# Kernel tuning notes

Measured on AMD Instinct MI355X. Metric: run time of the kernel, lower is better.

## Reference

```python
import jax, jax.numpy as jnp
import numpy as np

B, L, D, T = 32, 2048, 64, 512          # batch, seq_len, input_dim, pred steps
H, EK = 2, 64                           # num_heads, embed_dim_per_head
E = H * EK                              # embed_dim = 128
P = 2                                   # function 'L' -> 2 coefficients
LAT, HID = 64, 64                       # latent_dim, hidden_dim
DIM = 2 * D                             # value dim after cat(X, M)


def setup_inputs() -> dict:
    key = jax.random.key(0)
    ks = jax.random.split(key, 20)
    s = 0.05
    inp = {
        "timesteps": jnp.sort(jax.random.uniform(ks[0], (B, L)), axis=-1),
        "X": jax.random.normal(ks[1], (B, L, D)),
        "M": jax.random.bernoulli(ks[2], 0.5, (B, L, D)).astype(jnp.float32),
        "y_time_steps": jnp.sort(jax.random.uniform(ks[3], (B, T)), axis=-1),
        # time_embedding: Linear(1, E)
        "te_w": jax.random.normal(ks[4], (1, E)) * s,
        "te_b": jax.random.normal(ks[5], (E,)) * s,
        # learned queries (1, P, E)
        "query": jax.random.normal(ks[6], (1, P, E)),
        # query_map / key_map: Linear(E, E), stored (in, out)
        "qm_w": jax.random.normal(ks[7], (E, E)) * s,
        "qm_b": jax.random.normal(ks[8], (E,)) * s,
        "km_w": jax.random.normal(ks[9], (E, E)) * s,
        "km_b": jax.random.normal(ks[10], (E,)) * s,
        # shared attention output head: Linear(2*D*H, LAT)
        "out_w": jax.random.normal(ks[11], (DIM * H, LAT)) * s,
        "out_b": jax.random.normal(ks[12], (LAT,)) * s,
        # decoder (depth=1): Linear(LAT, HID) -> ReLU -> Linear(HID, D)
        "dec_w1": jax.random.normal(ks[13], (LAT, HID)) * s,
        "dec_b1": jax.random.normal(ks[14], (HID,)) * s,
        "dec_w2": jax.random.normal(ks[15], (HID, D)) * s,
        "dec_b2": jax.random.normal(ks[16], (D,)) * s,
    }
    return inp


def _forward(timesteps, X, M, y_time_steps, te_w, te_b, query,
             qm_w, qm_b, km_w, km_b, out_w, out_b,
             dec_w1, dec_b1, dec_w2, dec_b2):
    # learn_time_embedding: Linear(1,E) then sin() on indices i % H == 0
    te = timesteps[..., None] @ te_w + te_b                 # (B, L, E)
    sin_idx = (jnp.arange(E) % H) == 0
    key_emb = jnp.where(sin_idx, jnp.sin(te), te)           # (B, L, E)

    value = jnp.concatenate([X, M], axis=-1)                # (B, L, 2D)
    mask = jnp.concatenate([M, M], axis=-1)                 # (B, L, 2D)

    q = query @ qm_w + qm_b                                 # (1, P, E)
    k = key_emb @ km_w + km_b                               # (B, L, E)
    qh = q.reshape(1, P, H, EK).transpose(0, 2, 1, 3)       # (1, H, P, EK)
    kh = k.reshape(B, L, H, EK).transpose(0, 2, 1, 3)       # (B, H, L, EK)

    scores = jnp.einsum('xhpe,bhle->bhpl', qh, kh) / jnp.sqrt(jnp.float32(EK))
    # score broadcast over value dim + per-feature mask fill (-1e9 as in torch)
    logits = jnp.where(mask[:, None, None, :, :] == 0, -1e9,
                       scores[..., None])                   # (B, H, P, L, 2D)
    p_attn = jax.nn.softmax(logits, axis=-2)                # softmax over L
    x = jnp.einsum('bhpld,bld->bhpd', p_attn, value)        # (B, H, P, 2D)

    x = x.transpose(0, 2, 1, 3).reshape(B, P, H * DIM)      # (B, P, H*2D)
    coeffs = x @ out_w + out_b                              # (B, P, LAT)

    # function 'L': linear-in-time latent trajectory
    z = coeffs[:, 0, :][:, None, :] + y_time_steps[..., None] * coeffs[:, 1, :][:, None, :]  # (B, T, LAT)
    h1 = jax.nn.relu(z @ dec_w1 + dec_b1)
    out = h1 @ dec_w2 + dec_b2                              # (B, T, D)
    return out, coeffs


def reference(timesteps, X, M, y_time_steps, te_w, te_b, query,
              qm_w, qm_b, km_w, km_b, out_w, out_b,
              dec_w1, dec_b1, dec_w2, dec_b2):
    return _forward(timesteps, X, M, y_time_steps, te_w, te_b, query,
                    qm_w, qm_b, km_w, km_b, out_w, out_b,
                    dec_w1, dec_b1, dec_w2, dec_b2)
```

## Files before the change

### kernel.cpp

```cpp
#include <hip/hip_runtime.h>
#include <hip/hip_bf16.h>

#define BB 32
#define LL 2048
#define DD 64
#define TT 512

#define NCHUNK 16
#define PSTRIDE 576

__global__ void __launch_bounds__(256) k_attn(
    const float* __restrict__ ts,
    const float* __restrict__ X,
    const float* __restrict__ M,
    const float* __restrict__ te_w,
    const float* __restrict__ te_b,
    const float* __restrict__ query,
    const float* __restrict__ qm_w,
    const float* __restrict__ qm_b,
    const float* __restrict__ km_w,
    const float* __restrict__ km_b,
    float* __restrict__ ws) {
  __shared__ float q_lds[256];
  __shared__ float r_lds[512], c_lds[4];
  __shared__ float tew[128], teb[128];
  __shared__ float w_lds[128 * 4];
  __shared__ float red[256 * 18];
  const int t = threadIdx.x;
  const int b = blockIdx.y;
  const int lc = blockIdx.x * 128;

  if (t < 128) { tew[t] = te_w[t]; teb[t] = te_b[t]; }
  {
    const int p = t >> 7, e = t & 127;
    float acc = qm_b[e];
#pragma unroll 8
    for (int i = 0; i < 128; ++i)
      acc += query[p * 128 + i] * qm_w[i * 128 + e];
    q_lds[t] = acc;
  }
  __syncthreads();

  for (int o = t; o < 512; o += 256) {
    const int hp = o >> 7, i = o & 127;
    const int h = hp >> 1, p = hp & 1;
    const float4* km4 = (const float4*)(km_w + i * 128 + h * 64);
    const float* qp = &q_lds[p * 128 + h * 64];
    float acc = 0.f;
#pragma unroll
    for (int e4 = 0; e4 < 16; ++e4) {
      const float4 w = km4[e4];
      acc += qp[e4 * 4] * w.x + qp[e4 * 4 + 1] * w.y +
             qp[e4 * 4 + 2] * w.z + qp[e4 * 4 + 3] * w.w;
    }
    r_lds[o] = acc;
  }
  if (t < 4) {
    const int h = t >> 1, p = t & 1;
    float acc = 0.f;
    for (int e = 0; e < 64; ++e)
      acc += q_lds[p * 128 + h * 64 + e] * km_b[h * 64 + e];
    c_lds[t] = acc;
  }
  __syncthreads();

  {
    const int ll = t >> 1, pair = t & 1;
    const float tt = ts[(size_t)b * LL + lc + ll];
    float a0 = 0.f, a1 = 0.f;
    const float* r0 = &r_lds[(pair * 2) * 128];
    const float* r1 = &r_lds[(pair * 2 + 1) * 128];
    for (int i = 0; i < 128; i += 2) {
      const float f0 = __sinf(tt * tew[i] + teb[i]);
      const float f1 = tt * tew[i + 1] + teb[i + 1];
      a0 += f0 * r0[i] + f1 * r0[i + 1];
      a1 += f0 * r1[i] + f1 * r1[i + 1];
    }
    w_lds[ll * 4 + pair * 2]     = __expf((a0 + c_lds[pair * 2]) * 0.125f);
    w_lds[ll * 4 + pair * 2 + 1] = __expf((a1 + c_lds[pair * 2 + 1]) * 0.125f);
  }
  __syncthreads();

  const int dpair = t & 31, lr = t >> 5;
  float n[4][2] = {}, dn[4][2] = {}, sx[2] = {};
  const float2* X2 = (const float2*)X;
  const float2* M2 = (const float2*)M;
  const size_t base = ((size_t)b * LL + lc) * 32;
  for (int ll = lr; ll < 128; ll += 8) {
    const float2 xv = X2[base + (size_t)ll * 32 + dpair];
    const float2 mv = M2[base + (size_t)ll * 32 + dpair];
    const float mx0 = mv.x * xv.x, mx1 = mv.y * xv.y;
    sx[0] += xv.x; sx[1] += xv.y;
#pragma unroll
    for (int hp = 0; hp < 4; ++hp) {
      const float w = w_lds[ll * 4 + hp];
      n[hp][0]  += w * mx0;  n[hp][1]  += w * mx1;
      dn[hp][0] += w * mv.x; dn[hp][1] += w * mv.y;
    }
  }

#pragma unroll
  for (int hp = 0; hp < 4; ++hp) {
    red[t * 18 + hp * 2 + 0] = n[hp][0];
    red[t * 18 + hp * 2 + 1] = n[hp][1];
    red[t * 18 + 8 + hp * 2 + 0] = dn[hp][0];
    red[t * 18 + 8 + hp * 2 + 1] = dn[hp][1];
  }
  red[t * 18 + 16] = sx[0];
  red[t * 18 + 17] = sx[1];
  __syncthreads();

  if (t < 32) {
    float* slot = ws + ((size_t)b * NCHUNK + blockIdx.x) * PSTRIDE;
    for (int j = 0; j < 18; ++j) {
      float s = 0.f;
#pragma unroll
      for (int r2 = 0; r2 < 8; ++r2) s += red[(r2 * 32 + t) * 18 + j];
      if (j < 8) {
        const int hp = j >> 1, half = j & 1;
        slot[hp * 64 + 2 * t + half] = s;
      } else if (j < 16) {
        const int j2 = j - 8, hp = j2 >> 1, half = j2 & 1;
        slot[256 + hp * 64 + 2 * t + half] = s;
      } else {
        slot[512 + 2 * t + (j - 16)] = s;
      }
    }
  }
}

__global__ void __launch_bounds__(256) k_dec(
    const float* __restrict__ yts,
    const float* __restrict__ out_w,
    const float* __restrict__ out_b,
    const float* __restrict__ dec_w1,
    const float* __restrict__ dec_b1,
    const float* __restrict__ dec_w2,
    const float* __restrict__ dec_b2,
    const float* __restrict__ ws,
    float* __restrict__ out) {
  __shared__ float acc_l[576];
  __shared__ float x_lds[512];
  __shared__ float c_lds[128];
  __shared__ float ABl[128];
  __shared__ __align__(16) float w2l[4096];
  __shared__ float h1l[16 * 64];
  __shared__ float b2l[64], yl[64];
  const int t = threadIdx.x;
  const int b = blockIdx.y;
  const int t0 = blockIdx.x * 64;

  for (int i = t; i < 4096; i += 256) w2l[i] = dec_w2[i];
  {
    const float* p = ws + (size_t)b * NCHUNK * PSTRIDE;
    for (int o = t; o < 576; o += 256) {
      float s = 0.f;
#pragma unroll
      for (int c = 0; c < NCHUNK; ++c) s += p[c * PSTRIDE + o];
      acc_l[o] = s;
    }
  }
  if (t < 64) { b2l[t] = dec_b2[t]; yl[t] = yts[b * TT + t0 + t]; }
  __syncthreads();

  {
    const int hp = t >> 6, d = t & 63;
    const int h = hp >> 1, p = hp & 1;
    const float num = acc_l[hp * 64 + d];
    const float den = acc_l[256 + hp * 64 + d];
    const float sxv = acc_l[512 + d];
    float x1, x2;
    if (den > 0.f) { x1 = num / den; x2 = 1.f; }
    else           { x1 = sxv * (1.f / (float)LL); x2 = 0.f; }
    x_lds[p * 256 + h * 128 + d] = x1;
    x_lds[p * 256 + h * 128 + 64 + d] = x2;
  }
  __syncthreads();

  if (t < 128) {
    const int p = t >> 6, j = t & 63;
    float acc = out_b[j];
    for (int k = 0; k < 256; ++k)
      acc += x_lds[p * 256 + k] * out_w[k * 64 + j];
    c_lds[t] = acc;
    if (blockIdx.x == 0)
      out[(size_t)BB * TT * DD + b * 128 + t] = acc;
  }
  __syncthreads();

  if (t < 64) {
    const int k = t;
    float a = dec_b1[k], bb = 0.f;
    for (int j = 0; j < 64; ++j) {
      const float w1 = dec_w1[j * 64 + k];
      a  += c_lds[j] * w1;
      bb += c_lds[64 + j] * w1;
    }
    ABl[k] = a;
    ABl[64 + k] = bb;
  }
  __syncthreads();

  const int tl = t >> 4, dg = t & 15;
  for (int it = 0; it < 4; ++it) {
    {
      int idx = t;
#pragma unroll
      for (int rr = 0; rr < 4; ++rr, idx += 256) {
        const int tl2 = idx >> 6, k = idx & 63;
        h1l[idx] = fmaxf(ABl[k] + yl[it * 16 + tl2] * ABl[64 + k], 0.f);
      }
    }
    __syncthreads();
    {
      float a0 = b2l[dg * 4], a1 = b2l[dg * 4 + 1],
            a2 = b2l[dg * 4 + 2], a3 = b2l[dg * 4 + 3];
      const float4* w4 = (const float4*)w2l;
      const float* h1p = &h1l[tl * 64];
      for (int k = 0; k < 64; ++k) {
        const float h = h1p[k];
        const float4 w = w4[k * 16 + dg];
        a0 += h * w.x; a1 += h * w.y; a2 += h * w.z; a3 += h * w.w;
      }
      const int tg = t0 + it * 16 + tl;
      const size_t off = ((size_t)b * TT + tg) * 64 + dg * 4;
      float4 o; o.x = a0; o.y = a1; o.z = a2; o.w = a3;
      *(float4*)(out + off) = o;
    }
    __syncthreads();
  }
}

extern "C" void kernel_launch(void* const* d_in, const int* in_sizes, int n_in,
                              void* d_out, int out_size, void* d_ws, size_t ws_size,
                              hipStream_t stream) {
  const float* ts     = (const float*)d_in[0];
  const float* X      = (const float*)d_in[1];
  const float* M      = (const float*)d_in[2];
  const float* yts    = (const float*)d_in[3];
  const float* te_w   = (const float*)d_in[4];
  const float* te_b   = (const float*)d_in[5];
  const float* query  = (const float*)d_in[6];
  const float* qm_w   = (const float*)d_in[7];
  const float* qm_b   = (const float*)d_in[8];
  const float* km_w   = (const float*)d_in[9];
  const float* km_b   = (const float*)d_in[10];
  const float* out_w  = (const float*)d_in[11];
  const float* out_b  = (const float*)d_in[12];
  const float* dec_w1 = (const float*)d_in[13];
  const float* dec_b1 = (const float*)d_in[14];
  const float* dec_w2 = (const float*)d_in[15];
  const float* dec_b2 = (const float*)d_in[16];
  float* ws = (float*)d_ws;
  float* out = (float*)d_out;

  k_attn<<<dim3(NCHUNK, BB), 256, 0, stream>>>(
      ts, X, M, te_w, te_b, query, qm_w, qm_b, km_w, km_b, ws);
  k_dec<<<dim3(TT / 64, BB), 256, 0, stream>>>(
      yts, out_w, out_b, dec_w1, dec_b1, dec_w2, dec_b2, ws, out);
}
```

Baseline: 139.2 us.

## Fold linear time-embedding terms into constants, prefetch X/M, split decoder reductions

In the attention kernel, the linear (non-sin) half of the time embedding is folded algebraically into per-head constants C0/C1, so only the 64 sin features are evaluated per timestep. The sin uses the hardware sin builtin on inputs pre-scaled by 1/2π, and the work is split across two threads per row with an LDS reduction. The first half of X/M is loaded into registers before the score computation so the global loads overlap it. In the decoder kernel, the workspace reduction is vectorised with float4, and the out_w and dec_w1 matvecs are split across more threads with small LDS reductions. The changes add extra syncs and register pressure in exchange for less serial work.

Result: faster. 133.3 us, median of 2 (-4.2%).

```diff
diff --git a/kernel.cpp b/kernel.cpp
--- a/kernel.cpp
+++ b/kernel.cpp
@@ -5,6 +5,7 @@
 #define LL 2048
 #define DD 64
 #define TT 512
+#define INV2PI 0.15915494309189535f
 
 #define NCHUNK 16
 #define PSTRIDE 576
@@ -22,22 +23,47 @@
     const float* __restrict__ km_b,
     float* __restrict__ ws) {
   __shared__ float q_lds[256];
-  __shared__ float r_lds[512], c_lds[4];
-  __shared__ float tew[128], teb[128];
-  __shared__ float w_lds[128 * 4];
+  __shared__ float r_lds[512];
+  __shared__ __align__(16) float rp4[256];
+  __shared__ __align__(8)  float feat2[128];
+  __shared__ float tsl[128];
+  __shared__ float C0[4], C1[4];
+  __shared__ float sred[1024];
+  __shared__ float w_lds[512];
   __shared__ float red[256 * 18];
   const int t = threadIdx.x;
   const int b = blockIdx.y;
   const int lc = blockIdx.x * 128;
 
-  if (t < 128) { tew[t] = te_w[t]; teb[t] = te_b[t]; }
+  if (t < 128) tsl[t] = ts[(size_t)b * LL + lc + t];
+  if (t < 64) {
+    feat2[2 * t]     = te_w[2 * t] * INV2PI;
+    feat2[2 * t + 1] = te_b[2 * t] * INV2PI;
+  }
+
   {
     const int p = t >> 7, e = t & 127;
-    float acc = qm_b[e];
-#pragma unroll 8
-    for (int i = 0; i < 128; ++i)
-      acc += query[p * 128 + i] * qm_w[i * 128 + e];
-    q_lds[t] = acc;
+    const float* qq = query + p * 128;
+    const float* qw = qm_w + e;
+    float a0 = 0.f, a1 = 0.f, a2 = 0.f, a3 = 0.f;
+    for (int i = 0; i < 128; i += 4) {
+      a0 += qq[i]     * qw[i * 128];
+      a1 += qq[i + 1] * qw[(i + 1) * 128];
+      a2 += qq[i + 2] * qw[(i + 2) * 128];
+      a3 += qq[i + 3] * qw[(i + 3) * 128];
+    }
+    q_lds[t] = (a0 + a1) + (a2 + a3) + qm_b[e];
+  }
+
+  const int dpair = t & 31, lr = t >> 5;
+  const float2* X2 = (const float2*)X;
+  const float2* M2 = (const float2*)M;
+  const size_t base = ((size_t)b * LL + lc) * 32;
+  float2 xa[8], ma[8];
+#pragma unroll
+  for (int i = 0; i < 8; ++i) {
+    xa[i] = X2[base + (size_t)(lr + i * 8) * 32 + dpair];
+    ma[i] = M2[base + (size_t)(lr + i * 8) * 32 + dpair];
   }
   __syncthreads();
 
@@ -50,43 +76,80 @@
 #pragma unroll
     for (int e4 = 0; e4 < 16; ++e4) {
       const float4 w = km4[e4];
-      acc += qp[e4 * 4] * w.x + qp[e4 * 4 + 1] * w.y +
-             qp[e4 * 4 + 2] * w.z + qp[e4 * 4 + 3] * w.w;
+      acc += qp[4 * e4] * w.x + qp[4 * e4 + 1] * w.y +
+             qp[4 * e4 + 2] * w.z + qp[4 * e4 + 3] * w.w;
     }
     r_lds[o] = acc;
   }
-  if (t < 4) {
-    const int h = t >> 1, p = t & 1;
-    float acc = 0.f;
-    for (int e = 0; e < 64; ++e)
-      acc += q_lds[p * 128 + h * 64 + e] * km_b[h * 64 + e];
-    c_lds[t] = acc;
-  }
-  __syncthreads();
-
-  {
-    const int ll = t >> 1, pair = t & 1;
-    const float tt = ts[(size_t)b * LL + lc + ll];
-    float a0 = 0.f, a1 = 0.f;
-    const float* r0 = &r_lds[(pair * 2) * 128];
-    const float* r1 = &r_lds[(pair * 2 + 1) * 128];
-    for (int i = 0; i < 128; i += 2) {
-      const float f0 = __sinf(tt * tew[i] + teb[i]);
-      const float f1 = tt * tew[i + 1] + teb[i + 1];
-      a0 += f0 * r0[i] + f1 * r0[i + 1];
-      a1 += f0 * r1[i] + f1 * r1[i + 1];
-    }
-    w_lds[ll * 4 + pair * 2]     = __expf((a0 + c_lds[pair * 2]) * 0.125f);
-    w_lds[ll * 4 + pair * 2 + 1] = __expf((a1 + c_lds[pair * 2 + 1]) * 0.125f);
-  }
-  __syncthreads();
-
-  const int dpair = t & 31, lr = t >> 5;
+  __syncthreads();
+
+  if (t < 64) {
+#pragma unroll
+    for (int hp = 0; hp < 4; ++hp) rp4[t * 4 + hp] = r_lds[hp * 128 + 2 * t];
+  }
+  if (t >= 64 && t < 72) {
+    const int hp = (t - 64) >> 1;
+    if ((t & 1) == 0) {
+      float s = 0.f;
+      for (int e = 0; e < 64; ++e) s += te_w[2 * e + 1] * r_lds[hp * 128 + 2 * e + 1];
+      C1[hp] = s;
+    } else {
+      float s = 0.f;
+      for (int e = 0; e < 64; ++e) s += te_b[2 * e + 1] * r_lds[hp * 128 + 2 * e + 1];
+      const int h = hp >> 1, p = hp & 1;
+      float c = 0.f;
+      for (int e = 0; e < 64; ++e) c += q_lds[p * 128 + h * 64 + e] * km_b[h * 64 + e];
+      C0[hp] = s + c;
+    }
+  }
+  __syncthreads();
+
+  {
+    const int l = t >> 1, half = t & 1;
+    const float tt = tsl[l];
+    const float2* f2 = (const float2*)feat2;
+    const float4* r4 = (const float4*)rp4;
+    float p0 = 0.f, p1 = 0.f, p2 = 0.f, p3 = 0.f;
+    const int e0 = half * 32;
+    for (int e = e0; e < e0 + 32; ++e) {
+      const float2 wb = f2[e];
+      const float f = __builtin_amdgcn_sinf(tt * wb.x + wb.y);
+      const float4 r = r4[e];
+      p0 += f * r.x; p1 += f * r.y; p2 += f * r.z; p3 += f * r.w;
+    }
+    sred[t * 4 + 0] = p0; sred[t * 4 + 1] = p1;
+    sred[t * 4 + 2] = p2; sred[t * 4 + 3] = p3;
+  }
+  __syncthreads();
+  {
+    const int l = t >> 1, pr = t & 1;
+    const float tt = tsl[l];
+#pragma unroll
+    for (int k2 = 0; k2 < 2; ++k2) {
+      const int hp = pr * 2 + k2;
+      const float s = sred[(2 * l) * 4 + hp] + sred[(2 * l + 1) * 4 + hp] +
+                      tt * C1[hp] + C0[hp];
+      w_lds[l * 4 + hp] = __expf(s * 0.125f);
+    }
+  }
+  __syncthreads();
+
   float n[4][2] = {}, dn[4][2] = {}, sx[2] = {};
-  const float2* X2 = (const float2*)X;
-  const float2* M2 = (const float2*)M;
-  const size_t base = ((size_t)b * LL + lc) * 32;
-  for (int ll = lr; ll < 128; ll += 8) {
+#pragma unroll
+  for (int i = 0; i < 8; ++i) {
+    const int ll = lr + i * 8;
+    const float2 xv = xa[i], mv = ma[i];
+    const float mx0 = mv.x * xv.x, mx1 = mv.y * xv.y;
+    sx[0] += xv.x; sx[1] += xv.y;
+#pragma unroll
+    for (int hp = 0; hp < 4; ++hp) {
+      const float w = w_lds[ll * 4 + hp];
+      n[hp][0]  += w * mx0;  n[hp][1]  += w * mx1;
+      dn[hp][0] += w * mv.x; dn[hp][1] += w * mv.y;
+    }
+  }
+  for (int i = 8; i < 16; ++i) {
+    const int ll = lr + i * 8;
     const float2 xv = X2[base + (size_t)ll * 32 + dpair];
     const float2 mv = M2[base + (size_t)ll * 32 + dpair];
     const float mx0 = mv.x * xv.x, mx1 = mv.y * xv.y;
@@ -139,28 +202,38 @@
     const float* __restrict__ dec_b2,
     const float* __restrict__ ws,
     float* __restrict__ out) {
-  __shared__ float acc_l[576];
+  __shared__ __align__(16) float acc_l[576];
   __shared__ float x_lds[512];
+  __shared__ float cred[256];
   __shared__ float c_lds[128];
+  __shared__ float abred[256];
   __shared__ float ABl[128];
   __shared__ __align__(16) float w2l[4096];
-  __shared__ float h1l[16 * 64];
+  __shared__ float h1l[1024];
   __shared__ float b2l[64], yl[64];
   const int t = threadIdx.x;
   const int b = blockIdx.y;
   const int t0 = blockIdx.x * 64;
 
-  for (int i = t; i < 4096; i += 256) w2l[i] = dec_w2[i];
-  {
-    const float* p = ws + (size_t)b * NCHUNK * PSTRIDE;
-    for (int o = t; o < 576; o += 256) {
-      float s = 0.f;
-#pragma unroll
-      for (int c = 0; c < NCHUNK; ++c) s += p[c * PSTRIDE + o];
-      acc_l[o] = s;
-    }
-  }
-  if (t < 64) { b2l[t] = dec_b2[t]; yl[t] = yts[b * TT + t0 + t]; }
+  {
+    const float4* s4 = (const float4*)dec_w2;
+    float4* d4 = (float4*)w2l;
+    for (int i = t; i < 1024; i += 256) d4[i] = s4[i];
+  }
+  if (t < 144) {
+    const float4* p4 = (const float4*)(ws + (size_t)b * NCHUNK * PSTRIDE);
+    float4 s; s.x = s.y = s.z = s.w = 0.f;
+    for (int c = 0; c < NCHUNK; ++c) {
+      const float4 v = p4[(size_t)c * 144 + t];
+      s.x += v.x; s.y += v.y; s.z += v.z; s.w += v.w;
+    }
+    ((float4*)acc_l)[t] = s;
+  }
+  if (t >= 192) {
+    const int k = t - 192;
+    b2l[k] = dec_b2[k];
+    yl[k] = yts[b * TT + t0 + k];
+  }
   __syncthreads();
 
   {
@@ -177,27 +250,39 @@
   }
   __syncthreads();
 
+  {
+    const int kh = t >> 7, pj = t & 127, p = pj >> 6, j = pj & 63;
+    float acc = (kh == 0) ? out_b[j] : 0.f;
+    const float* xp = &x_lds[p * 256 + kh * 128];
+    const float* wp = out_w + (size_t)kh * 128 * 64 + j;
+    for (int k = 0; k < 128; ++k) acc += xp[k] * wp[k * 64];
+    cred[t] = acc;
+  }
+  __syncthreads();
   if (t < 128) {
-    const int p = t >> 6, j = t & 63;
-    float acc = out_b[j];
-    for (int k = 0; k < 256; ++k)
-      acc += x_lds[p * 256 + k] * out_w[k * 64 + j];
-    c_lds[t] = acc;
+    const float c = cred[t] + cred[t + 128];
+    c_lds[t] = c;
     if (blockIdx.x == 0)
-      out[(size_t)BB * TT * DD + b * 128 + t] = acc;
-  }
-  __syncthreads();
-
+      out[(size_t)BB * TT * DD + b * 128 + t] = c;
+  }
+  __syncthreads();
+  if (t < 128) {
+    const int jh = t >> 6, k = t & 63;
+    float a = 0.f, bb = 0.f;
+    const float* cp = &c_lds[jh * 32];
+    const float* cp2 = &c_lds[64 + jh * 32];
+    for (int j = 0; j < 32; ++j) {
+      const float w1 = dec_w1[(jh * 32 + j) * 64 + k];
+      a += cp[j] * w1;
+      bb += cp2[j] * w1;
+    }
+    abred[t * 2] = a;
+    abred[t * 2 + 1] = bb;
+  }
+  __syncthreads();
   if (t < 64) {
-    const int k = t;
-    float a = dec_b1[k], bb = 0.f;
-    for (int j = 0; j < 64; ++j) {
-      const float w1 = dec_w1[j * 64 + k];
-      a  += c_lds[j] * w1;
-      bb += c_lds[64 + j] * w1;
-    }
-    ABl[k] = a;
-    ABl[64 + k] = bb;
+    ABl[t]      = dec_b1[t] + abred[t * 2]     + abred[(64 + t) * 2];
+    ABl[64 + t] =             abred[t * 2 + 1] + abred[(64 + t) * 2 + 1];
   }
   __syncthreads();
 
```
